# Optimization experiments

Hardware: AMD Instinct MI355X
Metric: run time of the kernel (lower is better)

## Reference

```python
import jax, jax.numpy as jnp
import numpy as np

N, D, OUT, K = 1_000_000, 128, 128, 10
B2 = 4096            # final batch of nodes
B1 = B2 * K          # depth-1 frontier size


def setup_inputs() -> dict:
    key = jax.random.key(0)
    k1, k2, k3, k4, k5, k6, k7 = jax.random.split(key, 7)
    raw_features = jax.random.normal(k1, (N, D), dtype=jnp.float32)
    # SageLayer weights: [out, 2*in] (gcn=False => concat(self, agg))
    W1 = jax.random.normal(k2, (OUT, 2 * D), dtype=jnp.float32) * 0.05
    W2 = jax.random.normal(k3, (OUT, 2 * OUT), dtype=jnp.float32) * 0.05
    # depth-1 frontier node ids and their K sampled neighbors (global ids)
    nodes1 = jax.random.randint(k4, (B1,), 0, N)
    neigh1 = jax.random.randint(k5, (B1, K), 0, N)
    # batch nodes remapped to local indices into the depth-1 hidden table
    nodes2 = jax.random.randint(k6, (B2,), 0, B1)
    neigh2 = jax.random.randint(k7, (B2, K), 0, B1)
    return {"raw_features": raw_features, "W1": W1, "W2": W2,
            "nodes1": nodes1, "neigh1": neigh1,
            "nodes2": nodes2, "neigh2": neigh2}


def sage_layer(self_feats, agg_feats, W):
    # relu(concat(self, agg) @ W^T), matching SageLayer with gcn=False
    combined = jnp.concatenate([self_feats, agg_feats], axis=1)
    return jax.nn.relu(combined @ W.T)


def reference(raw_features, W1, W2, nodes1, neigh1, nodes2, neigh2):
    # Layer 1: mean-aggregate sampled neighbor raw features (gather + mean
    # replaces the dense mask.mm mean in the original).
    agg1 = jnp.mean(raw_features[neigh1], axis=1)      # [B1, D]
    h1 = sage_layer(raw_features[nodes1], agg1, W1)    # [B1, OUT]
    # Layer 2: neighbors indexed locally into the layer-1 hidden table
    agg2 = jnp.mean(h1[neigh2], axis=1)                # [B2, OUT]
    h2 = sage_layer(h1[nodes2], agg2, W2)              # [B2, OUT]
    return h2
```

## Files before the change

kernel.cpp:

```cpp
#include <hip/hip_runtime.h>


typedef __attribute__((ext_vector_type(8))) short  short8;
typedef __attribute__((ext_vector_type(8))) __bf16 bf16x8;
typedef __attribute__((ext_vector_type(4))) float  f32x4;

#define K_NEIGH 10
#define NB      32
#define PITCH   264

__device__ inline float b2f(short s) {
    union { unsigned int u; float f; } c;
    c.u = ((unsigned int)(unsigned short)s) << 16;
    return c.f;
}
__device__ inline short f2b(float f) {
    union { float f; unsigned int u; } c; c.f = f;
    unsigned int u = c.u;
    return (short)((u + 0x7fffu + ((u >> 16) & 1u)) >> 16);
}
__device__ inline bf16x8 as_bf16x8(short8 s) {
    union { short8 s; bf16x8 b; } c; c.s = s; return c.b;
}

__global__ void detect_f32(const unsigned short* __restrict__ w, int* __restrict__ flag) {
    if (threadIdx.x == 0 && blockIdx.x == 0) {
        int f = 0;
        for (int i = 0; i < 64; ++i) {
            unsigned int e = ((unsigned int)w[2 * i] >> 7) & 0xFFu;
            if (e >= 132u) f = 1;
        }
        *flag = f;
    }
}

__launch_bounds__(256, 2)
__global__ void sage_layer(const void* __restrict__ table,
                           const void* __restrict__ Wv,
                           const int*  __restrict__ nodes,
                           const int*  __restrict__ neigh,
                           void*       __restrict__ outv,
                           const int*  __restrict__ flag,
                           const int table_by_flag, const int out_by_flag)
{
    __shared__ __align__(16) short lds[NB * PITCH];
    const int t    = threadIdx.x;
    const int blk  = blockIdx.x;
    const int lane = t & 63;
    const int wave = t >> 6;
    const int n15  = lane & 15;
    const int q    = lane >> 4;
    const int f32in = *flag;
    const bool t32 = table_by_flag && f32in;
    const bool o32 = out_by_flag && f32in;

    short8 bfrag[2][8];
    if (!f32in) {
        const short* W = (const short*)Wv;
#pragma unroll
        for (int ot = 0; ot < 2; ++ot) {
            const int o = wave * 32 + ot * 16 + n15;
#pragma unroll
            for (int fk = 0; fk < 8; ++fk)
                bfrag[ot][fk] = *(const short8*)(W + o * 256 + fk * 32 + q * 8);
        }
    } else {
        const float* W = (const float*)Wv;
#pragma unroll
        for (int ot = 0; ot < 2; ++ot) {
            const int o = wave * 32 + ot * 16 + n15;
#pragma unroll
            for (int fk = 0; fk < 8; ++fk) {
                const float* p = W + o * 256 + fk * 32 + q * 8;
                f32x4 v0 = *(const f32x4*)p;
                f32x4 v1 = *(const f32x4*)(p + 4);
                short8 s;
#pragma unroll
                for (int i = 0; i < 4; ++i) { s[i] = f2b(v0[i]); s[4 + i] = f2b(v1[i]); }
                bfrag[ot][fk] = s;
            }
        }
    }

    {
        const int m    = t >> 3;
        const int part = t & 7;
        const int gi   = blk * NB + m;
        const int self_id = nodes[gi];
        short8 s0, s1;
        float a[16];
#pragma unroll
        for (int i = 0; i < 16; ++i) a[i] = 0.f;

        if (!t32) {
            const short* srow = (const short*)table + (long)self_id * 128 + part * 16;
            s0 = *(const short8*)(srow);
            s1 = *(const short8*)(srow + 8);
            for (int k = 0; k < K_NEIGH; ++k) {
                const int nid = neigh[gi * K_NEIGH + k];
                const short* nrow = (const short*)table + (long)nid * 128 + part * 16;
                short8 v0 = *(const short8*)(nrow);
                short8 v1 = *(const short8*)(nrow + 8);
#pragma unroll
                for (int i = 0; i < 8; ++i) { a[i] += b2f(v0[i]); a[8 + i] += b2f(v1[i]); }
            }
        } else {
            const float* srow = (const float*)table + (long)self_id * 128 + part * 16;
            f32x4 u0 = *(const f32x4*)(srow);
            f32x4 u1 = *(const f32x4*)(srow + 4);
            f32x4 u2 = *(const f32x4*)(srow + 8);
            f32x4 u3 = *(const f32x4*)(srow + 12);
#pragma unroll
            for (int i = 0; i < 4; ++i) {
                s0[i] = f2b(u0[i]); s0[4 + i] = f2b(u1[i]);
                s1[i] = f2b(u2[i]); s1[4 + i] = f2b(u3[i]);
            }
            for (int k = 0; k < K_NEIGH; ++k) {
                const int nid = neigh[gi * K_NEIGH + k];
                const float* nrow = (const float*)table + (long)nid * 128 + part * 16;
                f32x4 v0 = *(const f32x4*)(nrow);
                f32x4 v1 = *(const f32x4*)(nrow + 4);
                f32x4 v2 = *(const f32x4*)(nrow + 8);
                f32x4 v3 = *(const f32x4*)(nrow + 12);
#pragma unroll
                for (int i = 0; i < 4; ++i) {
                    a[i] += v0[i]; a[4 + i] += v1[i]; a[8 + i] += v2[i]; a[12 + i] += v3[i];
                }
            }
        }
        short8 g0, g1;
#pragma unroll
        for (int i = 0; i < 8; ++i) { g0[i] = f2b(a[i] * 0.1f); g1[i] = f2b(a[8 + i] * 0.1f); }
        short* dst = lds + m * PITCH + part * 16;
        *(short8*)(dst)       = s0;
        *(short8*)(dst + 8)   = s1;
        *(short8*)(dst + 128) = g0;
        *(short8*)(dst + 136) = g1;
    }
    __syncthreads();

    f32x4 acc[2][2] = {};
#pragma unroll
    for (int mb = 0; mb < 2; ++mb) {
        const short* arow = lds + (mb * 16 + n15) * PITCH + q * 8;
        short8 af[8];
#pragma unroll
        for (int fk = 0; fk < 8; ++fk) af[fk] = *(const short8*)(arow + fk * 32);
#pragma unroll
        for (int ot = 0; ot < 2; ++ot)
#pragma unroll
            for (int fk = 0; fk < 8; ++fk)
                acc[mb][ot] = __builtin_amdgcn_mfma_f32_16x16x32_bf16(
                    as_bf16x8(af[fk]), as_bf16x8(bfrag[ot][fk]), acc[mb][ot], 0, 0, 0);
    }

#pragma unroll
    for (int mb = 0; mb < 2; ++mb)
#pragma unroll
        for (int ot = 0; ot < 2; ++ot) {
            const int col = wave * 32 + ot * 16 + n15;
#pragma unroll
            for (int r = 0; r < 4; ++r) {
                const long row = blk * NB + mb * 16 + q * 4 + r;
                float v = acc[mb][ot][r];
                v = v > 0.f ? v : 0.f;
                if (!o32) ((short*)outv)[row * 128 + col] = f2b(v);
                else      ((float*)outv)[row * 128 + col] = v;
            }
        }
}

extern "C" void kernel_launch(void* const* d_in, const int* in_sizes, int n_in,
                              void* d_out, int out_size, void* d_ws, size_t ws_size,
                              hipStream_t stream) {
    const void* raw    = d_in[0];
    const void* W1     = d_in[1];
    const void* W2     = d_in[2];
    const int*  nodes1 = (const int*)d_in[3];
    const int*  neigh1 = (const int*)d_in[4];
    const int*  nodes2 = (const int*)d_in[5];
    const int*  neigh2 = (const int*)d_in[6];

    int*   flag = (int*)d_ws;
    short* h1   = (short*)((char*)d_ws + 256);

    const int B1 = in_sizes[3];
    const int B2 = in_sizes[5];

    detect_f32<<<1, 64, 0, stream>>>((const unsigned short*)W1, flag);
    sage_layer<<<B1 / NB, 256, 0, stream>>>(raw, W1, nodes1, neigh1, h1, flag,
                                            1, 0);
    sage_layer<<<B2 / NB, 256, 0, stream>>>(h1, W2, nodes2, neigh2, d_out, flag,
                                            0, 1);
}
```

Before: 623.1 us.

## Split layer-1 into a gather-aggregate kernel and a separate GEMM kernel

Layer 1 is split in two. A light gather kernel, launched with higher occupancy (launch bounds 4) and with its neighbor indices preloaded and the loop fully unrolled, writes the concatenated self and mean rows to a bf16 workspace buffer. A separate MFMA GEMM kernel then reads that buffer. The aim is more memory-level parallelism for the random row gathers, which the fused kernel limited by holding weight fragments in registers at 2 blocks per CU. The cost is an extra round trip through global memory of roughly 21 MB, plus one more launch. Layer 2 also gets the index preload and unrolled loop.

```diff
diff --git a/kernel.cpp b/kernel.cpp
--- a/kernel.cpp
+++ b/kernel.cpp
@@ -32,6 +32,169 @@
         }
         *flag = f;
     }
+}
+
+__launch_bounds__(256, 4)
+__global__ void gather_agg(const void* __restrict__ table,
+                           const int*  __restrict__ nodes,
+                           const int*  __restrict__ neigh,
+                           short*      __restrict__ comb,
+                           const int*  __restrict__ flag,
+                           const int table_by_flag)
+{
+    const int idx  = blockIdx.x * 256 + threadIdx.x;
+    const int node = idx >> 3;
+    const int part = idx & 7;
+    const bool t32 = table_by_flag && *flag;
+
+    const int self_id = nodes[node];
+    int nid[K_NEIGH];
+#pragma unroll
+    for (int k = 0; k < K_NEIGH; ++k) nid[k] = neigh[node * K_NEIGH + k];
+
+    short8 s0, s1;
+    float a[16];
+#pragma unroll
+    for (int i = 0; i < 16; ++i) a[i] = 0.f;
+
+    if (!t32) {
+        const short* base = (const short*)table;
+        const short* srow = base + (long)self_id * 128 + part * 16;
+        s0 = *(const short8*)(srow);
+        s1 = *(const short8*)(srow + 8);
+#pragma unroll
+        for (int k = 0; k < K_NEIGH; ++k) {
+            const short* nrow = base + (long)nid[k] * 128 + part * 16;
+            short8 v0 = *(const short8*)(nrow);
+            short8 v1 = *(const short8*)(nrow + 8);
+#pragma unroll
+            for (int i = 0; i < 8; ++i) { a[i] += b2f(v0[i]); a[8 + i] += b2f(v1[i]); }
+        }
+    } else {
+        const float* base = (const float*)table;
+        const float* srow = base + (long)self_id * 128 + part * 16;
+        f32x4 u0 = *(const f32x4*)(srow);
+        f32x4 u1 = *(const f32x4*)(srow + 4);
+        f32x4 u2 = *(const f32x4*)(srow + 8);
+        f32x4 u3 = *(const f32x4*)(srow + 12);
+#pragma unroll
+        for (int i = 0; i < 4; ++i) {
+            s0[i] = f2b(u0[i]); s0[4 + i] = f2b(u1[i]);
+            s1[i] = f2b(u2[i]); s1[4 + i] = f2b(u3[i]);
+        }
+#pragma unroll
+        for (int k = 0; k < K_NEIGH; ++k) {
+            const float* nrow = base + (long)nid[k] * 128 + part * 16;
+            f32x4 v0 = *(const f32x4*)(nrow);
+            f32x4 v1 = *(const f32x4*)(nrow + 4);
+            f32x4 v2 = *(const f32x4*)(nrow + 8);
+            f32x4 v3 = *(const f32x4*)(nrow + 12);
+#pragma unroll
+            for (int i = 0; i < 4; ++i) {
+                a[i] += v0[i]; a[4 + i] += v1[i]; a[8 + i] += v2[i]; a[12 + i] += v3[i];
+            }
+        }
+    }
+    short8 g0, g1;
+#pragma unroll
+    for (int i = 0; i < 8; ++i) { g0[i] = f2b(a[i] * 0.1f); g1[i] = f2b(a[8 + i] * 0.1f); }
+    short* dst = comb + (long)node * 256 + part * 16;
+    *(short8*)(dst)       = s0;
+    *(short8*)(dst + 8)   = s1;
+    *(short8*)(dst + 128) = g0;
+    *(short8*)(dst + 136) = g1;
+}
+
+__launch_bounds__(256, 2)
+__global__ void gemm_combined(const short* __restrict__ comb,
+                              const void* __restrict__ Wv,
+                              void*       __restrict__ outv,
+                              const int*  __restrict__ flag,
+                              const int out_by_flag)
+{
+    __shared__ __align__(16) short lds[NB * PITCH];
+    const int t    = threadIdx.x;
+    const int blk  = blockIdx.x;
+    const int lane = t & 63;
+    const int wave = t >> 6;
+    const int n15  = lane & 15;
+    const int q    = lane >> 4;
+    const int f32in = *flag;
+    const bool o32 = out_by_flag && f32in;
+
+    short8 bfrag[2][8];
+    if (!f32in) {
+        const short* W = (const short*)Wv;
+#pragma unroll
+        for (int ot = 0; ot < 2; ++ot) {
+            const int o = wave * 32 + ot * 16 + n15;
+#pragma unroll
+            for (int fk = 0; fk < 8; ++fk)
+                bfrag[ot][fk] = *(const short8*)(W + o * 256 + fk * 32 + q * 8);
+        }
+    } else {
+        const float* W = (const float*)Wv;
+#pragma unroll
+        for (int ot = 0; ot < 2; ++ot) {
+            const int o = wave * 32 + ot * 16 + n15;
+#pragma unroll
+            for (int fk = 0; fk < 8; ++fk) {
+                const float* p = W + o * 256 + fk * 32 + q * 8;
+                f32x4 v0 = *(const f32x4*)p;
+                f32x4 v1 = *(const f32x4*)(p + 4);
+                short8 s;
+#pragma unroll
+                for (int i = 0; i < 4; ++i) { s[i] = f2b(v0[i]); s[4 + i] = f2b(v1[i]); }
+                bfrag[ot][fk] = s;
+            }
+        }
+    }
+
+    {
+        const int m   = t >> 3;
+        const int col = (t & 7) * 32;
+        const short* src = comb + (long)blk * (NB * 256) + m * 256 + col;
+        short8 x0 = *(const short8*)(src);
+        short8 x1 = *(const short8*)(src + 8);
+        short8 x2 = *(const short8*)(src + 16);
+        short8 x3 = *(const short8*)(src + 24);
+        short* dst = lds + m * PITCH + col;
+        *(short8*)(dst)      = x0;
+        *(short8*)(dst + 8)  = x1;
+        *(short8*)(dst + 16) = x2;
+        *(short8*)(dst + 24) = x3;
+    }
+    __syncthreads();
+
+    f32x4 acc[2][2] = {};
+#pragma unroll
+    for (int mb = 0; mb < 2; ++mb) {
+        const short* arow = lds + (mb * 16 + n15) * PITCH + q * 8;
+        short8 af[8];
+#pragma unroll
+        for (int fk = 0; fk < 8; ++fk) af[fk] = *(const short8*)(arow + fk * 32);
+#pragma unroll
+        for (int ot = 0; ot < 2; ++ot)
+#pragma unroll
+            for (int fk = 0; fk < 8; ++fk)
+                acc[mb][ot] = __builtin_amdgcn_mfma_f32_16x16x32_bf16(
+                    as_bf16x8(af[fk]), as_bf16x8(bfrag[ot][fk]), acc[mb][ot], 0, 0, 0);
+    }
+
+#pragma unroll
+    for (int mb = 0; mb < 2; ++mb)
+#pragma unroll
+        for (int ot = 0; ot < 2; ++ot) {
+            const int col = wave * 32 + ot * 16 + n15;
+#pragma unroll
+            for (int r = 0; r < 4; ++r) {
+                const long row = blk * NB + mb * 16 + q * 4 + r;
+                float v = acc[mb][ot][r];
+                v = v > 0.f ? v : 0.f;
+                if (!o32) ((short*)outv)[row * 128 + col] = f2b(v);
+                else      ((float*)outv)[row * 128 + col] = v;
+            }
+        }
 }
 
 __launch_bounds__(256, 2)
@@ -87,6 +250,9 @@
         const int part = t & 7;
         const int gi   = blk * NB + m;
         const int self_id = nodes[gi];
+        int nidv[K_NEIGH];
+#pragma unroll
+        for (int k = 0; k < K_NEIGH; ++k) nidv[k] = neigh[gi * K_NEIGH + k];
         short8 s0, s1;
         float a[16];
 #pragma unroll
@@ -96,9 +262,9 @@
             const short* srow = (const short*)table + (long)self_id * 128 + part * 16;
             s0 = *(const short8*)(srow);
             s1 = *(const short8*)(srow + 8);
+#pragma unroll
             for (int k = 0; k < K_NEIGH; ++k) {
-                const int nid = neigh[gi * K_NEIGH + k];
-                const short* nrow = (const short*)table + (long)nid * 128 + part * 16;
+                const short* nrow = (const short*)table + (long)nidv[k] * 128 + part * 16;
                 short8 v0 = *(const short8*)(nrow);
                 short8 v1 = *(const short8*)(nrow + 8);
 #pragma unroll
@@ -115,9 +281,9 @@
                 s0[i] = f2b(u0[i]); s0[4 + i] = f2b(u1[i]);
                 s1[i] = f2b(u2[i]); s1[4 + i] = f2b(u3[i]);
             }
+#pragma unroll
             for (int k = 0; k < K_NEIGH; ++k) {
-                const int nid = neigh[gi * K_NEIGH + k];
-                const float* nrow = (const float*)table + (long)nid * 128 + part * 16;
+                const float* nrow = (const float*)table + (long)nidv[k] * 128 + part * 16;
                 f32x4 v0 = *(const f32x4*)(nrow);
                 f32x4 v1 = *(const f32x4*)(nrow + 4);
                 f32x4 v2 = *(const f32x4*)(nrow + 8);
@@ -183,13 +349,15 @@
 
     int*   flag = (int*)d_ws;
     short* h1   = (short*)((char*)d_ws + 256);
+    short* comb = (short*)((char*)d_ws + 256 + 10485760);
 
     const int B1 = in_sizes[3];
     const int B2 = in_sizes[5];
 
     detect_f32<<<1, 64, 0, stream>>>((const unsigned short*)W1, flag);
-    sage_layer<<<B1 / NB, 256, 0, stream>>>(raw, W1, nodes1, neigh1, h1, flag,
-                                            1, 0);
+    gather_agg<<<(B1 * 8) / 256, 256, 0, stream>>>(raw, nodes1, neigh1, comb, flag,
+                                                   1);
+    gemm_combined<<<B1 / NB, 256, 0, stream>>>(comb, W1, h1, flag, 0);
     sage_layer<<<B2 / NB, 256, 0, stream>>>(h1, W2, nodes2, neigh2, d_out, flag,
                                             0, 1);
 }
```

After: 635.0 us. About the same (+1.9%).
